# Kernel optimization log

Measured on AMD Instinct MI355X. Metric: run time of the kernel, lower is better.

## Reference

```python
import jax, jax.numpy as jnp
import numpy as np

B, L, D, N_ITEMS = 512, 100, 128, 100000
ALPHA = 0.3


def setup_inputs() -> dict:
    key = jax.random.key(0)
    ks = jax.random.split(key, 10)
    x = jax.random.randint(ks[0], (B, L), 0, N_ITEMS, dtype=jnp.int32)
    attn_mask = jnp.ones((B, L), dtype=bool)  # unused by forward (parity with torch signature)
    emb = jax.random.normal(ks[1], (N_ITEMS, D), dtype=jnp.float32) * 0.02
    emb = emb.at[0].set(0.0)  # padding_idx=0 row is zeros
    s = 1.0 / np.sqrt(D)
    W_in = jax.random.uniform(ks[2], (D, D), minval=-s, maxval=s, dtype=jnp.float32)
    W_out = jax.random.uniform(ks[3], (D, D), minval=-s, maxval=s, dtype=jnp.float32)
    w_ih = jax.random.uniform(ks[4], (3 * D, D), minval=-s, maxval=s, dtype=jnp.float32)
    w_hh = jax.random.uniform(ks[5], (3 * D, D), minval=-s, maxval=s, dtype=jnp.float32)
    b_ih = jax.random.uniform(ks[6], (3 * D,), minval=-s, maxval=s, dtype=jnp.float32)
    b_hh = jax.random.uniform(ks[7], (3 * D,), minval=-s, maxval=s, dtype=jnp.float32)
    sr = 1.0 / np.sqrt(3 * D)
    W_read = jax.random.uniform(ks[8], (D, 3 * D), minval=-sr, maxval=sr, dtype=jnp.float32)
    b_read = jax.random.uniform(ks[9], (D,), minval=-sr, maxval=sr, dtype=jnp.float32)
    return dict(x=x, attn_mask=attn_mask, emb=emb, W_in=W_in, W_out=W_out,
                w_ih=w_ih, w_hh=w_hh, b_ih=b_ih, b_hh=b_hh, W_read=W_read, b_read=b_read)


def _forward(x, emb, W_in, W_out, w_ih, w_hh, b_ih, b_hh, W_read, b_read):
    n_items, d = emb.shape
    seq_len = x.shape[1]
    BIG = n_items  # sentinel > any item id
    NEG = -1e9

    def per_sample(seq):
        valid = seq != 0
        cnt = valid.sum()
        # --- torch.unique(nonzero, return_inverse=True) via sort + dedup ---
        s = jnp.where(valid, seq, BIG)
        ss = jnp.sort(s)
        prev = jnp.concatenate([jnp.full((1,), -1, ss.dtype), ss[:-1]])
        is_first = (ss != prev) & (ss != BIG)
        n_nodes = is_first.sum()
        rank = jnp.cumsum(is_first) - 1
        nodes_s = jnp.full((seq_len,), BIG, ss.dtype).at[
            jnp.where(is_first, rank, seq_len)].set(ss, mode='drop')  # sorted unique ids, BIG-padded
        node_mask = jnp.arange(seq_len) < n_nodes
        nodes = jnp.where(node_mask, nodes_s, 0)  # pad slots -> item 0 (zero emb row)
        inv = jnp.searchsorted(nodes_s, s)  # inverse indices for valid positions
        # compact nonzero items preserving order (for consecutive-pair edges)
        pos = jnp.cumsum(valid) - 1
        cidx = jnp.where(valid, pos, seq_len)
        compact_inv = jnp.zeros((seq_len,), inv.dtype).at[cidx].set(inv, mode='drop')
        compact_seq = jnp.zeros((seq_len,), seq.dtype).at[cidx].set(seq, mode='drop')
        last_tok = compact_seq[jnp.maximum(cnt - 1, 0)]
        src, dst = compact_inv[:-1], compact_inv[1:]
        edge_mask = jnp.arange(seq_len - 1) < cnt - 1
        # --- message passing: index_add + degree normalize ---
        H0 = emb[nodes]  # [L, d]
        Hin = H0 @ W_in.T
        Hout = H0 @ W_out.T
        dst_safe = jnp.where(edge_mask, dst, seq_len)
        agg = jnp.zeros((seq_len, d), H0.dtype).at[dst_safe].add(
            jnp.where(edge_mask[:, None], Hout[src], 0.0), mode='drop')
        deg = jnp.zeros((seq_len,), H0.dtype).at[dst_safe].add(1.0, mode='drop')
        deg = jnp.maximum(deg, 1.0)
        xin = Hin + agg / deg[:, None]
        # --- GRUCell(xin, H0), torch gate order (r, z, n) ---
        gi = xin @ w_ih.T + b_ih
        gh = H0 @ w_hh.T + b_hh
        gi_r, gi_z, gi_n = jnp.split(gi, 3, axis=-1)
        gh_r, gh_z, gh_n = jnp.split(gh, 3, axis=-1)
        r = jax.nn.sigmoid(gi_r + gh_r)
        z = jax.nn.sigmoid(gi_z + gh_z)
        nct = jnp.tanh(gi_n + r * gh_n)
        H = (1.0 - z) * nct + z * H0
        H = jnp.where(node_mask[:, None], H, 0.0)  # drop padded node slots
        # --- attention readout anchored at last item ---
        li = jnp.clip(jnp.searchsorted(nodes_s, last_tok), 0, seq_len - 1)
        h_last = H[li]
        scores = jnp.where(node_mask, H @ h_last, NEG)
        att = jax.nn.softmax(scores)
        local = att @ H
        gvec = jnp.zeros((d,), H.dtype)  # cooc is None -> zeros_like(local)
        h_read = jnp.tanh(W_read @ jnp.concatenate([h_last, local, ALPHA * gvec]) + b_read)
        row = h_read @ emb.T  # tied output weights
        default = jnp.full((n_items,), NEG, row.dtype).at[0].set(0.0)
        return jnp.where(cnt >= 2, row, default)

    return jax.vmap(per_sample)(x)


def reference(x, attn_mask, emb, W_in, W_out, w_ih, w_hh, b_ih, b_hh, W_read, b_read):
    return _forward(x, emb, W_in, W_out, w_ih, w_hh, b_ih, b_hh, W_read, b_read)
```

## Files before the change

kernel.cpp:

```cpp
#include <hip/hip_runtime.h>
#include <math.h>

#define BATCH 512
#define SEQL  100
#define DIM   128
#define NITEMS 100000
#define NEGV  -1000000000.0f

#define OFF_WPACK_F 0
#define OFF_WREADT  147456
#define OFF_APACK_F 196608
#define OFF_HBUF    262144
#define OFF_GD      6815744
#define OFF_EPACK_F 13369344
#define OFF_NODES_I 26173440
#define OFF_SRC_I   26224640
#define OFF_DST_I   26275328
#define OFF_INFO_I  26326016

typedef __attribute__((ext_vector_type(8))) short bf16x8;
typedef __attribute__((ext_vector_type(4))) short s16x4;
typedef __attribute__((ext_vector_type(4))) float f32x4;

__device__ __forceinline__ unsigned short bf16_rne(float x) {
  unsigned int u = __float_as_uint(x);
  unsigned int r = u + 0x7FFFu + ((u >> 16) & 1u);
  return (unsigned short)(r >> 16);
}
__device__ __forceinline__ float bf16_to_f(unsigned short h) {
  return __uint_as_float(((unsigned int)h) << 16);
}

__global__ __launch_bounds__(256) void k_pack(
    const float* __restrict__ emb, const float* __restrict__ w_ih,
    const float* __restrict__ w_hh, const float* __restrict__ W_in,
    const float* __restrict__ W_out, const float* __restrict__ W_read,
    float* __restrict__ WreadT, unsigned short* __restrict__ wpack,
    unsigned short* __restrict__ epack) {
  int bid = blockIdx.x, tid = threadIdx.x;
  if (bid < 6252) {
    int idx = bid * 256 + tid;
    int lane = idx & 63;
    int kc = (idx >> 6) & 3;
    int it = idx >> 8;
    int quad = lane >> 4, rr = lane & 15;
    int row = it * 16 + rr;
    int kbase = kc * 32 + quad * 8;
    float4 v0 = {0.f, 0.f, 0.f, 0.f}, v1 = {0.f, 0.f, 0.f, 0.f};
    if (row < NITEMS) {
      const float4* p = (const float4*)(emb + (size_t)row * 128 + kbase);
      v0 = p[0]; v1 = p[1];
    }
    float vs[8] = {v0.x, v0.y, v0.z, v0.w, v1.x, v1.y, v1.z, v1.w};
    bf16x8 hi, lo;
    #pragma unroll
    for (int j = 0; j < 8; ++j) {
      unsigned short h = bf16_rne(vs[j]);
      hi[j] = (short)h;
      lo[j] = (short)bf16_rne(vs[j] - bf16_to_f(h));
    }
    size_t base = ((size_t)(it * 4 + kc) * 2) * 512 + (size_t)lane * 8;
    *(bf16x8*)&epack[base] = hi;
    *(bf16x8*)&epack[base + 512] = lo;
  } else if (bid < 6828) {
    int idx = (bid - 6252) * 256 + tid;
    int mat = idx / 49152, rem = idx % 49152;
    int n = rem >> 7, k = rem & 127;
    float v;
    if (mat == 2) {
      v = w_hh[rem];
    } else {
      const float* Wx = mat ? W_out : W_in;
      const float* wr = w_ih + n * 128;
      float s = 0.f;
      for (int m = 0; m < 128; ++m) s = fmaf(wr[m], Wx[m * 128 + k], s);
      v = s;
    }
    unsigned short hi = bf16_rne(v);
    unsigned short lo = bf16_rne(v - bf16_to_f(hi));
    int nt = n >> 4, nn2 = n & 15, c = k >> 5, quad = (k >> 3) & 3, j = k & 7;
    int lane = quad * 16 + nn2;
    size_t base = ((size_t)((mat * 24 + nt) * 4 + c)) * 1024 + (size_t)lane * 8 + j;
    wpack[base] = hi;
    wpack[base + 512] = lo;
  } else {
    int idx = (bid - 6828) * 256 + tid;
    int i = idx / 384, jj = idx % 384;
    WreadT[jj * 128 + i] = W_read[idx];
  }
}

__global__ void k_build(const int* __restrict__ x, int* __restrict__ nodes,
                        int* __restrict__ esrc, int* __restrict__ edst,
                        int* __restrict__ info) {
  int b = blockIdx.x, tid = threadIdx.x;
  __shared__ int sseq[SEQL];
  __shared__ unsigned char sisf[SEQL];
  __shared__ int srank[SEQL];
  __shared__ int scinv[SEQL];
  __shared__ int snodes[SEQL];
  __shared__ int s_nn, s_cnt;
  if (tid < SEQL) { sseq[tid] = x[b * SEQL + tid]; snodes[tid] = 0; }
  __syncthreads();
  int t = (tid < SEQL) ? sseq[tid] : 0;
  bool valid = (tid < SEQL) && (t != 0);
  int f = tid;
  if (valid) {
    for (int j = 0; j < tid; ++j) if (sseq[j] == t) { f = j; break; }
  }
  int isf = (valid && f == tid) ? 1 : 0;
  if (tid < SEQL) sisf[tid] = (unsigned char)isf;
  __syncthreads();
  int rank = 0, pos = 0;
  if (tid < SEQL) {
    for (int i = 0; i < tid; ++i) {
      rank += sisf[i];
      pos += (sseq[i] != 0) ? 1 : 0;
    }
    srank[tid] = rank;
    if (tid == SEQL - 1) { s_nn = rank + isf; s_cnt = pos + (valid ? 1 : 0); }
  }
  __syncthreads();
  if (valid) scinv[pos] = srank[f];
  if (isf) snodes[rank] = t;
  __syncthreads();
  int nn = s_nn, cnt = s_cnt;
  int ec = (cnt >= 2) ? cnt - 1 : 0;
  if (tid < ec) {
    esrc[b * 99 + tid] = scinv[tid];
    edst[b * 99 + tid] = scinv[tid + 1];
  }
  if (tid == 0) {
    info[b * 4 + 0] = ec;
    info[b * 4 + 1] = (cnt >= 1) ? scinv[cnt - 1] : 0;
    info[b * 4 + 2] = (cnt >= 2) ? 1 : 0;
    info[b * 4 + 3] = nn;
  }
  if (tid < SEQL) nodes[b * SEQL + tid] = snodes[tid];
}

__global__ __launch_bounds__(256) void k_agg(
    const float* __restrict__ emb, const int* __restrict__ nodes,
    const int* __restrict__ esrc, const int* __restrict__ edst,
    const int* __restrict__ info, float* __restrict__ Gd) {
  __shared__ float agg[SEQL * DIM];
  __shared__ float sdeg[SEQL];
  int b = blockIdx.x, tid = threadIdx.x;
  float4* a4 = (float4*)agg;
  for (int e = tid; e < SEQL * 32; e += 256) a4[e] = (float4){0.f, 0.f, 0.f, 0.f};
  if (tid < SEQL) sdeg[tid] = 0.f;
  __syncthreads();
  int ec = info[b * 4 + 0];
  if (tid < ec) atomicAdd(&sdeg[edst[b * 99 + tid]], 1.f);
  for (int idx = tid; idx < ec * DIM; idx += 256) {
    int e = idx >> 7, k = idx & 127;
    int tok = nodes[b * SEQL + esrc[b * 99 + e]];
    atomicAdd(&agg[edst[b * 99 + e] * DIM + k], emb[(size_t)tok * DIM + k]);
  }
  __syncthreads();
  for (int idx = tid; idx < SEQL * DIM; idx += 256) {
    int n = idx >> 7;
    Gd[((size_t)b * SEQL) * DIM + idx] = agg[idx] * (1.f / fmaxf(sdeg[n], 1.f));
  }
}

#define GPAD 136
__global__ __launch_bounds__(128) void k_gru(
    const float* __restrict__ emb, const int* __restrict__ nodes,
    const unsigned short* __restrict__ wpack, const float* __restrict__ Gd,
    const float* __restrict__ b_ih, const float* __restrict__ b_hh,
    const int* __restrict__ info, float* __restrict__ Hbuf) {
  __shared__ unsigned short Xhi[64 * GPAD];
  __shared__ unsigned short Xlo[64 * GPAD];
  __shared__ unsigned short Hhi[64 * GPAD];
  __shared__ unsigned short Hlo[64 * GPAD];
  int tid = threadIdx.x;
  int rowbase = blockIdx.x * 64;
  const float4* emb4 = (const float4*)emb;
  const float4* gd4 = (const float4*)Gd;
  for (int e = tid; e < 64 * 32; e += 128) {
    int r = e >> 5, c4 = e & 31;
    int row = rowbase + r;
    float4 xv = gd4[(size_t)row * 32 + c4];
    int tok = nodes[row];
    float4 hv = emb4[(size_t)tok * 32 + c4];
    int base = r * GPAD + c4 * 4;
    float xs[4] = {xv.x, xv.y, xv.z, xv.w};
    float hs[4] = {hv.x, hv.y, hv.z, hv.w};
    s16x4 xh, xl, hh, hl;
    #pragma unroll
    for (int q = 0; q < 4; ++q) {
      unsigned short h1 = bf16_rne(xs[q]);
      xh[q] = (short)h1; xl[q] = (short)bf16_rne(xs[q] - bf16_to_f(h1));
      unsigned short h2 = bf16_rne(hs[q]);
      hh[q] = (short)h2; hl[q] = (short)bf16_rne(hs[q] - bf16_to_f(h2));
    }
    *(s16x4*)&Xhi[base] = xh; *(s16x4*)&Xlo[base] = xl;
    *(s16x4*)&Hhi[base] = hh; *(s16x4*)&Hlo[base] = hl;
  }
  __syncthreads();
  int wave = tid >> 6, lane = tid & 63;
  int quad = lane >> 4, nIdx = lane & 15;
  int grows[2][4]; int zm[2][4];
  #pragma unroll
  for (int m = 0; m < 2; ++m)
    #pragma unroll
    for (int i = 0; i < 4; ++i) {
      int grow = rowbase + (wave * 2 + m) * 16 + quad * 4 + i;
      grows[m][i] = grow;
      int bs = grow / SEQL;
      int n = grow - bs * SEQL;
      zm[m][i] = (n < info[bs * 4 + 3]) ? 1 : 0;
    }

  for (int t = 0; t < 8; ++t) {
    f32x4 acc[2][3][2];
    #pragma unroll
    for (int m = 0; m < 2; ++m)
      #pragma unroll
      for (int g = 0; g < 3; ++g)
        #pragma unroll
        for (int p = 0; p < 2; ++p) acc[m][g][p] = (f32x4){0.f, 0.f, 0.f, 0.f};

    #pragma unroll
    for (int c = 0; c < 4; ++c) {
      bf16x8 aX[2][2], aH[2][2];
      #pragma unroll
      for (int m = 0; m < 2; ++m) {
        int off = ((wave * 2 + m) * 16 + nIdx) * GPAD + c * 32 + quad * 8;
        aX[m][0] = *(const bf16x8*)&Xhi[off];
        aX[m][1] = *(const bf16x8*)&Xlo[off];
        aH[m][0] = *(const bf16x8*)&Hhi[off];
        aH[m][1] = *(const bf16x8*)&Hlo[off];
      }
      #pragma unroll
      for (int g = 0; g < 3; ++g) {
        size_t base1 = ((size_t)((0 * 24 + g * 8 + t) * 4 + c)) * 1024 + (size_t)lane * 8;
        size_t base2 = ((size_t)((1 * 24 + g * 8 + t) * 4 + c)) * 1024 + (size_t)lane * 8;
        size_t base3 = ((size_t)((2 * 24 + g * 8 + t) * 4 + c)) * 1024 + (size_t)lane * 8;
        bf16x8 B1h = *(const bf16x8*)&wpack[base1];
        bf16x8 B1l = *(const bf16x8*)&wpack[base1 + 512];
        bf16x8 B2h = *(const bf16x8*)&wpack[base2];
        bf16x8 B2l = *(const bf16x8*)&wpack[base2 + 512];
        bf16x8 B3h = *(const bf16x8*)&wpack[base3];
        bf16x8 B3l = *(const bf16x8*)&wpack[base3 + 512];
        #pragma unroll
        for (int m = 0; m < 2; ++m) {
          acc[m][g][0] = __builtin_amdgcn_mfma_f32_16x16x32_bf16(aH[m][0], B1h, acc[m][g][0], 0, 0, 0);
          acc[m][g][0] = __builtin_amdgcn_mfma_f32_16x16x32_bf16(aX[m][0], B2h, acc[m][g][0], 0, 0, 0);
          acc[m][g][1] = __builtin_amdgcn_mfma_f32_16x16x32_bf16(aH[m][0], B3h, acc[m][g][1], 0, 0, 0);
          acc[m][g][0] = __builtin_amdgcn_mfma_f32_16x16x32_bf16(aH[m][1], B1h, acc[m][g][0], 0, 0, 0);
          acc[m][g][0] = __builtin_amdgcn_mfma_f32_16x16x32_bf16(aX[m][1], B2h, acc[m][g][0], 0, 0, 0);
          acc[m][g][1] = __builtin_amdgcn_mfma_f32_16x16x32_bf16(aH[m][1], B3h, acc[m][g][1], 0, 0, 0);
          acc[m][g][0] = __builtin_amdgcn_mfma_f32_16x16x32_bf16(aH[m][0], B1l, acc[m][g][0], 0, 0, 0);
          acc[m][g][0] = __builtin_amdgcn_mfma_f32_16x16x32_bf16(aX[m][0], B2l, acc[m][g][0], 0, 0, 0);
          acc[m][g][1] = __builtin_amdgcn_mfma_f32_16x16x32_bf16(aH[m][0], B3l, acc[m][g][1], 0, 0, 0);
        }
      }
    }
    int j = t * 16 + nIdx;
    float biR = b_ih[j],       bhR = b_hh[j];
    float biZ = b_ih[128 + j], bhZ = b_hh[128 + j];
    float biN = b_ih[256 + j], bhN = b_hh[256 + j];
    #pragma unroll
    for (int m = 0; m < 2; ++m)
      #pragma unroll
      for (int i = 0; i < 4; ++i) {
        float gr = acc[m][0][0][i] + biR + acc[m][0][1][i] + bhR;
        float gz = acc[m][1][0][i] + biZ + acc[m][1][1][i] + bhZ;
        float r = 1.f / (1.f + expf(-gr));
        float z = 1.f / (1.f + expf(-gz));
        float nct = tanhf(acc[m][2][0][i] + biN + r * (acc[m][2][1][i] + bhN));
        int lrow = (wave * 2 + m) * 16 + quad * 4 + i;
        float h0 = bf16_to_f(Hhi[lrow * GPAD + j]) + bf16_to_f(Hlo[lrow * GPAD + j]);
        float h = (1.f - z) * nct + z * h0;
        if (!zm[m][i]) h = 0.f;
        Hbuf[(size_t)grows[m][i] * 128 + j] = h;
      }
  }
}

#define HLS 129
__global__ void k_attn(const float* __restrict__ Hbuf, const float* __restrict__ WrT,
                       const float* __restrict__ b_read, const int* __restrict__ info,
                       unsigned short* __restrict__ apack) {
  int b = blockIdx.x, tid = threadIdx.x;
  __shared__ float Hl[SEQL * HLS];
  __shared__ float sc[128];
  __shared__ float hl[128];
  __shared__ float att[SEQL];
  __shared__ float loc[128];
  __shared__ float redm[2], reds[2];
  int nn = info[b * 4 + 3], li = info[b * 4 + 1];
  for (int e = tid; e < SEQL * 128; e += 128) {
    int r = e >> 7, k = e & 127;
    Hl[r * HLS + k] = Hbuf[((size_t)(b * SEQL + r)) * DIM + k];
  }
  __syncthreads();
  hl[tid] = Hl[li * HLS + tid];
  __syncthreads();
  float scr = NEGV;
  if (tid < nn) {
    float s = 0.f;
    for (int k = 0; k < 128; ++k) s += Hl[tid * HLS + k] * hl[k];
    scr = s;
  }
  sc[tid] = scr;
  __syncthreads();
  float m = sc[tid];
  #pragma unroll
  for (int o = 32; o >= 1; o >>= 1) m = fmaxf(m, __shfl_xor(m, o, 64));
  if ((tid & 63) == 0) redm[tid >> 6] = m;
  __syncthreads();
  m = fmaxf(redm[0], redm[1]);
  float e = (tid < SEQL) ? expf(sc[tid] - m) : 0.f;
  float s = e;
  #pragma unroll
  for (int o = 32; o >= 1; o >>= 1) s += __shfl_xor(s, o, 64);
  if ((tid & 63) == 0) reds[tid >> 6] = s;
  __syncthreads();
  float inv = 1.f / (reds[0] + reds[1]);
  if (tid < SEQL) att[tid] = e * inv;
  __syncthreads();
  float lv = 0.f;
  for (int n = 0; n < SEQL; ++n) lv = fmaf(att[n], Hl[n * HLS + tid], lv);
  loc[tid] = lv;
  __syncthreads();
  float acc = b_read[tid];
  for (int j = 0; j < 128; ++j) acc = fmaf(WrT[j * 128 + tid], hl[j], acc);
  for (int j = 0; j < 128; ++j) acc = fmaf(WrT[(128 + j) * 128 + tid], loc[j], acc);
  float hr = tanhf(acc);
  int mt = b >> 4, rr = b & 15;
  int kc = tid >> 5, q2 = (tid >> 3) & 3, j2 = tid & 7;
  unsigned short hi = bf16_rne(hr);
  unsigned short lo = bf16_rne(hr - bf16_to_f(hi));
  size_t base = ((size_t)(mt * 4 + kc) * 2) * 512 + (size_t)(q2 * 16 + rr) * 8 + j2;
  apack[base] = hi;
  apack[base + 512] = lo;
}

__global__ __launch_bounds__(256) void k_out(
    const unsigned short* __restrict__ epack, const unsigned short* __restrict__ apack,
    const int* __restrict__ info, float* __restrict__ out) {
  int tid = threadIdx.x;
  int wave = tid >> 6, lane = tid & 63;
  int quad = lane >> 4, nIdx = lane & 15;
  int b0   = blockIdx.x * 128;
  int itt0 = blockIdx.y * 4;
  int btg0 = blockIdx.x * 8 + wave * 2;

  bf16x8 bh[2][4], bl[2][4];
  #pragma unroll
  for (int m2 = 0; m2 < 2; ++m2)
    #pragma unroll
    for (int kc = 0; kc < 4; ++kc) {
      size_t base = ((size_t)((btg0 + m2) * 4 + kc) * 2) * 512 + (size_t)lane * 8;
      bh[m2][kc] = *(const bf16x8*)&apack[base];
      bl[m2][kc] = *(const bf16x8*)&apack[base + 512];
    }

  f32x4 acc[4][2];
  #pragma unroll
  for (int it = 0; it < 4; ++it)
    #pragma unroll
    for (int m2 = 0; m2 < 2; ++m2) acc[it][m2] = (f32x4){0.f, 0.f, 0.f, 0.f};

  #pragma unroll
  for (int it = 0; it < 4; ++it) {
    #pragma unroll
    for (int kc = 0; kc < 4; ++kc) {
      size_t abase = ((size_t)((itt0 + it) * 4 + kc) * 2) * 512 + (size_t)lane * 8;
      bf16x8 Ah = *(const bf16x8*)&epack[abase];
      bf16x8 Al = *(const bf16x8*)&epack[abase + 512];
      acc[it][0] = __builtin_amdgcn_mfma_f32_16x16x32_bf16(Ah, bh[0][kc], acc[it][0], 0, 0, 0);
      acc[it][1] = __builtin_amdgcn_mfma_f32_16x16x32_bf16(Ah, bh[1][kc], acc[it][1], 0, 0, 0);
      acc[it][0] = __builtin_amdgcn_mfma_f32_16x16x32_bf16(Al, bh[0][kc], acc[it][0], 0, 0, 0);
      acc[it][1] = __builtin_amdgcn_mfma_f32_16x16x32_bf16(Al, bh[1][kc], acc[it][1], 0, 0, 0);
      acc[it][0] = __builtin_amdgcn_mfma_f32_16x16x32_bf16(Ah, bl[0][kc], acc[it][0], 0, 0, 0);
      acc[it][1] = __builtin_amdgcn_mfma_f32_16x16x32_bf16(Ah, bl[1][kc], acc[it][1], 0, 0, 0);
    }
  }

  #pragma unroll
  for (int m2 = 0; m2 < 2; ++m2) {
    int b = b0 + (wave * 2 + m2) * 16 + nIdx;
    int flag = info[b * 4 + 2];
    #pragma unroll
    for (int it = 0; it < 4; ++it) {
      int ib = (itt0 + it) * 16 + quad * 4;
      if (ib < NITEMS) {
        float4 v;
        if (flag) {
          v.x = acc[it][m2][0]; v.y = acc[it][m2][1];
          v.z = acc[it][m2][2]; v.w = acc[it][m2][3];
        } else {
          v.x = (ib == 0) ? 0.f : NEGV; v.y = NEGV; v.z = NEGV; v.w = NEGV;
        }
        *(float4*)&out[(size_t)b * NITEMS + ib] = v;
      }
    }
  }
}

extern "C" void kernel_launch(void* const* d_in, const int* in_sizes, int n_in,
                              void* d_out, int out_size, void* d_ws, size_t ws_size,
                              hipStream_t stream) {
  const int*   x      = (const int*)d_in[0];
  const float* emb    = (const float*)d_in[2];
  const float* W_in   = (const float*)d_in[3];
  const float* W_out  = (const float*)d_in[4];
  const float* w_ih   = (const float*)d_in[5];
  const float* w_hh   = (const float*)d_in[6];
  const float* b_ih   = (const float*)d_in[7];
  const float* b_hh   = (const float*)d_in[8];
  const float* W_read = (const float*)d_in[9];
  const float* b_read = (const float*)d_in[10];
  float* ws  = (float*)d_ws;
  int*   wsi = (int*)d_ws;
  unsigned short* wpack  = (unsigned short*)(ws + OFF_WPACK_F);
  float*          WreadT = ws + OFF_WREADT;
  unsigned short* apack  = (unsigned short*)(ws + OFF_APACK_F);
  float*          Hbuf   = ws + OFF_HBUF;
  float*          GdBuf  = ws + OFF_GD;
  unsigned short* epack  = (unsigned short*)(ws + OFF_EPACK_F);
  int*            nodes  = wsi + OFF_NODES_I;
  int*            esrc   = wsi + OFF_SRC_I;
  int*            edst   = wsi + OFF_DST_I;
  int*            info   = wsi + OFF_INFO_I;
  float* out = (float*)d_out;

  k_pack<<<7020, 256, 0, stream>>>(emb, w_ih, w_hh, W_in, W_out, W_read,
                                   WreadT, wpack, epack);
  k_build<<<BATCH, 128, 0, stream>>>(x, nodes, esrc, edst, info);
  k_agg<<<BATCH, 256, 0, stream>>>(emb, nodes, esrc, edst, info, GdBuf);
  k_gru<<<800, 128, 0, stream>>>(emb, nodes, wpack, GdBuf, b_ih, b_hh, info, Hbuf);
  k_attn<<<BATCH, 128, 0, stream>>>(Hbuf, WreadT, b_read, info, apack);
  k_out<<<dim3(4, 1563), 256, 0, stream>>>(epack, apack, info, out);
}
```

Baseline: 524.1 us.

## Fuse graph build with aggregation and split GRU gate tiles across four waves

The build and aggregation kernels are merged into one, so the edge source/destination arrays stay in shared memory and are no longer written to and re-read from global memory, which also removes one launch. The GRU kernel goes from 128 to 256 threads per block, with each pair of waves handling half of the output column tiles, doubling the waves that work on each 64-row tile. The cost is more shared memory per build block and redundant A-fragment loads across the wave halves.

```diff
diff --git a/kernel.cpp b/kernel.cpp
--- a/kernel.cpp
+++ b/kernel.cpp
@@ -10,13 +10,11 @@
 #define OFF_WPACK_F 0
 #define OFF_WREADT  147456
 #define OFF_APACK_F 196608
-#define OFF_HBUF    262144
-#define OFF_GD      6815744
+#define OFF_GD      262144
+#define OFF_HBUF    6815744
 #define OFF_EPACK_F 13369344
 #define OFF_NODES_I 26173440
-#define OFF_SRC_I   26224640
-#define OFF_DST_I   26275328
-#define OFF_INFO_I  26326016
+#define OFF_INFO_I  26224640
 
 typedef __attribute__((ext_vector_type(8))) short bf16x8;
 typedef __attribute__((ext_vector_type(4))) short s16x4;
@@ -90,17 +88,26 @@
   }
 }
 
-__global__ void k_build(const int* __restrict__ x, int* __restrict__ nodes,
-                        int* __restrict__ esrc, int* __restrict__ edst,
-                        int* __restrict__ info) {
-  int b = blockIdx.x, tid = threadIdx.x;
+__global__ __launch_bounds__(256) void k_build_agg(
+    const int* __restrict__ x, const float* __restrict__ emb,
+    int* __restrict__ nodes, int* __restrict__ info, float* __restrict__ Gd) {
+  __shared__ float agg[SEQL * DIM];
+  __shared__ float sdeg[SEQL];
   __shared__ int sseq[SEQL];
   __shared__ unsigned char sisf[SEQL];
   __shared__ int srank[SEQL];
   __shared__ int scinv[SEQL];
   __shared__ int snodes[SEQL];
   __shared__ int s_nn, s_cnt;
-  if (tid < SEQL) { sseq[tid] = x[b * SEQL + tid]; snodes[tid] = 0; }
+  int b = blockIdx.x, tid = threadIdx.x;
+
+  if (tid < SEQL) {
+    sseq[tid] = x[b * SEQL + tid];
+    snodes[tid] = 0;
+    sdeg[tid] = 0.f;
+  }
+  float4* a4 = (float4*)agg;
+  for (int e = tid; e < SEQL * 32; e += 256) a4[e] = (float4){0.f, 0.f, 0.f, 0.f};
   __syncthreads();
   int t = (tid < SEQL) ? sseq[tid] : 0;
   bool valid = (tid < SEQL) && (t != 0);
@@ -124,38 +131,20 @@
   if (valid) scinv[pos] = srank[f];
   if (isf) snodes[rank] = t;
   __syncthreads();
-  int nn = s_nn, cnt = s_cnt;
+  int cnt = s_cnt;
   int ec = (cnt >= 2) ? cnt - 1 : 0;
-  if (tid < ec) {
-    esrc[b * 99 + tid] = scinv[tid];
-    edst[b * 99 + tid] = scinv[tid + 1];
-  }
+  if (tid < ec) atomicAdd(&sdeg[scinv[tid + 1]], 1.f);
   if (tid == 0) {
     info[b * 4 + 0] = ec;
     info[b * 4 + 1] = (cnt >= 1) ? scinv[cnt - 1] : 0;
     info[b * 4 + 2] = (cnt >= 2) ? 1 : 0;
-    info[b * 4 + 3] = nn;
+    info[b * 4 + 3] = s_nn;
   }
   if (tid < SEQL) nodes[b * SEQL + tid] = snodes[tid];
-}
-
-__global__ __launch_bounds__(256) void k_agg(
-    const float* __restrict__ emb, const int* __restrict__ nodes,
-    const int* __restrict__ esrc, const int* __restrict__ edst,
-    const int* __restrict__ info, float* __restrict__ Gd) {
-  __shared__ float agg[SEQL * DIM];
-  __shared__ float sdeg[SEQL];
-  int b = blockIdx.x, tid = threadIdx.x;
-  float4* a4 = (float4*)agg;
-  for (int e = tid; e < SEQL * 32; e += 256) a4[e] = (float4){0.f, 0.f, 0.f, 0.f};
-  if (tid < SEQL) sdeg[tid] = 0.f;
-  __syncthreads();
-  int ec = info[b * 4 + 0];
-  if (tid < ec) atomicAdd(&sdeg[edst[b * 99 + tid]], 1.f);
   for (int idx = tid; idx < ec * DIM; idx += 256) {
     int e = idx >> 7, k = idx & 127;
-    int tok = nodes[b * SEQL + esrc[b * 99 + e]];
-    atomicAdd(&agg[edst[b * 99 + e] * DIM + k], emb[(size_t)tok * DIM + k]);
+    int tok = snodes[scinv[e]];
+    atomicAdd(&agg[scinv[e + 1] * DIM + k], emb[(size_t)tok * DIM + k]);
   }
   __syncthreads();
   for (int idx = tid; idx < SEQL * DIM; idx += 256) {
@@ -165,7 +154,7 @@
 }
 
 #define GPAD 136
-__global__ __launch_bounds__(128) void k_gru(
+__global__ __launch_bounds__(256) void k_gru(
     const float* __restrict__ emb, const int* __restrict__ nodes,
     const unsigned short* __restrict__ wpack, const float* __restrict__ Gd,
     const float* __restrict__ b_ih, const float* __restrict__ b_hh,
@@ -178,7 +167,7 @@
   int rowbase = blockIdx.x * 64;
   const float4* emb4 = (const float4*)emb;
   const float4* gd4 = (const float4*)Gd;
-  for (int e = tid; e < 64 * 32; e += 128) {
+  for (int e = tid; e < 64 * 32; e += 256) {
     int r = e >> 5, c4 = e & 31;
     int row = rowbase + r;
     float4 xv = gd4[(size_t)row * 32 + c4];
@@ -199,35 +188,36 @@
     *(s16x4*)&Hhi[base] = hh; *(s16x4*)&Hlo[base] = hl;
   }
   __syncthreads();
-  int wave = tid >> 6, lane = tid & 63;
+  int w = tid >> 6, lane = tid & 63;
+  int p = w & 1, h = w >> 1;
   int quad = lane >> 4, nIdx = lane & 15;
   int grows[2][4]; int zm[2][4];
   #pragma unroll
   for (int m = 0; m < 2; ++m)
     #pragma unroll
     for (int i = 0; i < 4; ++i) {
-      int grow = rowbase + (wave * 2 + m) * 16 + quad * 4 + i;
+      int grow = rowbase + (p * 2 + m) * 16 + quad * 4 + i;
       grows[m][i] = grow;
       int bs = grow / SEQL;
       int n = grow - bs * SEQL;
       zm[m][i] = (n < info[bs * 4 + 3]) ? 1 : 0;
     }
 
-  for (int t = 0; t < 8; ++t) {
+  for (int t = h * 4; t < h * 4 + 4; ++t) {
     f32x4 acc[2][3][2];
     #pragma unroll
     for (int m = 0; m < 2; ++m)
       #pragma unroll
       for (int g = 0; g < 3; ++g)
         #pragma unroll
-        for (int p = 0; p < 2; ++p) acc[m][g][p] = (f32x4){0.f, 0.f, 0.f, 0.f};
+        for (int q = 0; q < 2; ++q) acc[m][g][q] = (f32x4){0.f, 0.f, 0.f, 0.f};
 
     #pragma unroll
     for (int c = 0; c < 4; ++c) {
       bf16x8 aX[2][2], aH[2][2];
       #pragma unroll
       for (int m = 0; m < 2; ++m) {
-        int off = ((wave * 2 + m) * 16 + nIdx) * GPAD + c * 32 + quad * 8;
+        int off = ((p * 2 + m) * 16 + nIdx) * GPAD + c * 32 + quad * 8;
         aX[m][0] = *(const bf16x8*)&Xhi[off];
         aX[m][1] = *(const bf16x8*)&Xlo[off];
         aH[m][0] = *(const bf16x8*)&Hhi[off];
@@ -271,11 +261,11 @@
         float r = 1.f / (1.f + expf(-gr));
         float z = 1.f / (1.f + expf(-gz));
         float nct = tanhf(acc[m][2][0][i] + biN + r * (acc[m][2][1][i] + bhN));
-        int lrow = (wave * 2 + m) * 16 + quad * 4 + i;
+        int lrow = (p * 2 + m) * 16 + quad * 4 + i;
         float h0 = bf16_to_f(Hhi[lrow * GPAD + j]) + bf16_to_f(Hlo[lrow * GPAD + j]);
-        float h = (1.f - z) * nct + z * h0;
-        if (!zm[m][i]) h = 0.f;
-        Hbuf[(size_t)grows[m][i] * 128 + j] = h;
+        float hv = (1.f - z) * nct + z * h0;
+        if (!zm[m][i]) hv = 0.f;
+        Hbuf[(size_t)grows[m][i] * 128 + j] = hv;
       }
   }
 }
@@ -420,20 +410,17 @@
   unsigned short* wpack  = (unsigned short*)(ws + OFF_WPACK_F);
   float*          WreadT = ws + OFF_WREADT;
   unsigned short* apack  = (unsigned short*)(ws + OFF_APACK_F);
+  float*          GdBuf  = ws + OFF_GD;
   float*          Hbuf   = ws + OFF_HBUF;
-  float*          GdBuf  = ws + OFF_GD;
   unsigned short* epack  = (unsigned short*)(ws + OFF_EPACK_F);
   int*            nodes  = wsi + OFF_NODES_I;
-  int*            esrc   = wsi + OFF_SRC_I;
-  int*            edst   = wsi + OFF_DST_I;
   int*            info   = wsi + OFF_INFO_I;
   float* out = (float*)d_out;
 
   k_pack<<<7020, 256, 0, stream>>>(emb, w_ih, w_hh, W_in, W_out, W_read,
                                    WreadT, wpack, epack);
-  k_build<<<BATCH, 128, 0, stream>>>(x, nodes, esrc, edst, info);
-  k_agg<<<BATCH, 256, 0, stream>>>(emb, nodes, esrc, edst, info, GdBuf);
-  k_gru<<<800, 128, 0, stream>>>(emb, nodes, wpack, GdBuf, b_ih, b_hh, info, Hbuf);
+  k_build_agg<<<BATCH, 256, 0, stream>>>(x, emb, nodes, info, GdBuf);
+  k_gru<<<800, 256, 0, stream>>>(emb, nodes, wpack, GdBuf, b_ih, b_hh, info, Hbuf);
   k_attn<<<BATCH, 128, 0, stream>>>(Hbuf, WreadT, b_read, info, apack);
   k_out<<<dim3(4, 1563), 256, 0, stream>>>(epack, apack, info, out);
 }
```

After: 534.4 us. About the same (+2.0%).
